# Performance work log

Measured on AMD Instinct MI355X. Metric: run time of the kernel, lower is better.

## Reference

```python
import jax, jax.numpy as jnp
import numpy as np

B, A, D, F, BF = 256, 128, 8, 512, 16  # batch, max_atoms, max_degree, atom_feat, bond_feat


def setup_inputs() -> dict:
    key = jax.random.key(0)
    k1, k2, k3 = jax.random.split(key, 3)
    atoms = jax.random.normal(k1, (B, A, F), dtype=jnp.float32)
    bonds = jax.random.normal(k2, (B, A, D, BF), dtype=jnp.float32)
    # -1 is the padding value for missing neighbours (as in the original layer)
    edges = jax.random.randint(k3, (B, A, D), -1, A, dtype=jnp.int32)
    return {"atoms": atoms, "bonds": bonds, "edges": edges}


def reference(atoms, bonds, edges):
    # atoms: (B, A, F); edges: (B, A, D) with -1 padding; bonds unused by this layer
    b, a, f = atoms.shape
    # neighbour_lookup with maskvalue=-inf: prepend a -inf row so index 0 (= edge -1 + 1) maps to mask
    pad = jnp.full((b, 1, f), -jnp.inf, dtype=atoms.dtype)
    masked_atoms = jnp.concatenate([pad, atoms], axis=1)        # (B, A+1, F)
    masked_edges = edges + 1                                     # (B, A, D), in [0, A]
    neigh = masked_atoms[jnp.arange(b)[:, None, None], masked_edges]  # (B, A, D, F)
    # include_self=True: prepend each atom's own features
    all_feats = jnp.concatenate([atoms[:, :, None, :], neigh], axis=2)  # (B, A, D+1, F)
    max_features = jnp.max(all_feats, axis=2)                   # (B, A, F)
    atom_degrees = jnp.sum(edges != -1, axis=-1, keepdims=True)  # (B, A, 1)
    general_atom_mask = (atom_degrees != 0).astype(atoms.dtype)
    return max_features * general_atom_mask
```

## Files before the change

kernel.cpp:

```cpp
#include <hip/hip_runtime.h>

#define B_ 256
#define A_ 128
#define D_ 8
#define F_ 512
#define NXCD 8

typedef float  vfloat4 __attribute__((ext_vector_type(4)));
typedef int    vint4   __attribute__((ext_vector_type(4)));

__global__ __launch_bounds__(128) void NeuralGraphPool_kernel(
    const float* __restrict__ atoms,
    const int*   __restrict__ edges,
    float*       __restrict__ out)
{
    const int hw  = blockIdx.x;
    const int blk = (hw & (NXCD - 1)) * ((B_ * A_) / NXCD) + (hw >> 3);

    const int b   = blk >> 7;
    const int a   = blk & (A_ - 1);
    const int t   = threadIdx.x;
    const int col = t * 4;

    const float* __restrict__ abase = atoms + (size_t)b * (A_ * F_);

    const int* ep = edges + (size_t)blk * D_;
    const vint4 e01 = *reinterpret_cast<const vint4*>(ep);
    const vint4 e23 = *reinterpret_cast<const vint4*>(ep + 4);
    int e[D_] = { e01.x, e01.y, e01.z, e01.w, e23.x, e23.y, e23.z, e23.w };

    int degree = 0;
#pragma unroll
    for (int d = 0; d < D_; ++d) degree += (e[d] >= 0) ? 1 : 0;

    vfloat4 acc = *reinterpret_cast<const vfloat4*>(abase + a * F_ + col);

#pragma unroll
    for (int d = 0; d < D_; ++d) {
        const int row = (e[d] >= 0) ? e[d] : a;
        const vfloat4 v = *reinterpret_cast<const vfloat4*>(abase + row * F_ + col);
        acc.x = fmaxf(acc.x, v.x);
        acc.y = fmaxf(acc.y, v.y);
        acc.z = fmaxf(acc.z, v.z);
        acc.w = fmaxf(acc.w, v.w);
    }

    vfloat4 r = acc;
    if (degree == 0) { r = (vfloat4)(0.f); }
    __builtin_nontemporal_store(r, reinterpret_cast<vfloat4*>(out + (size_t)blk * F_ + col));
}

extern "C" void kernel_launch(void* const* d_in, const int* in_sizes, int n_in,
                              void* d_out, int out_size, void* d_ws, size_t ws_size,
                              hipStream_t stream) {
    const float* atoms = (const float*)d_in[0];
    const int*   edges = (const int*)d_in[2];
    float*       out   = (float*)d_out;

    dim3 grid(B_ * A_);
    dim3 block(128);
    hipLaunchKernelGGL(NeuralGraphPool_kernel, grid, block, 0, stream,
                       atoms, edges, out);
}
```

Measured before the change: 31.01 us.

## Stage per-molecule feature slabs in LDS and gather neighbours from shared memory

Each block now handles one molecule and a 64-feature column chunk. It copies that 128x64 slab of atoms, plus the molecule's edge list, into shared memory, then computes the neighbour max for all atoms from LDS. Before, every atom block gathered up to 9 rows from global memory (mostly L2 hits), so this removes redundant global reads. In exchange it adds a __syncthreads, uses about 36KB of LDS per block, which limits occupancy, and may cause LDS bank conflicts from the irregular row gathers.

```diff
diff --git a/kernel.cpp b/kernel.cpp
--- a/kernel.cpp
+++ b/kernel.cpp
@@ -4,50 +4,77 @@
 #define A_ 128
 #define D_ 8
 #define F_ 512
+#define FC 64
+#define NCHUNK (F_ / FC)
+#define THREADS 256
 #define NXCD 8
 
-typedef float  vfloat4 __attribute__((ext_vector_type(4)));
-typedef int    vint4   __attribute__((ext_vector_type(4)));
+typedef float vfloat4 __attribute__((ext_vector_type(4)));
+typedef int   vint4   __attribute__((ext_vector_type(4)));
 
-__global__ __launch_bounds__(128) void NeuralGraphPool_kernel(
+__global__ __launch_bounds__(THREADS) void NeuralGraphPool_kernel(
     const float* __restrict__ atoms,
     const int*   __restrict__ edges,
     float*       __restrict__ out)
 {
+    __shared__ float slab[A_ * FC];
+    __shared__ int   eds[A_ * D_];
+
     const int hw  = blockIdx.x;
-    const int blk = (hw & (NXCD - 1)) * ((B_ * A_) / NXCD) + (hw >> 3);
+    const int blk = (hw & (NXCD - 1)) * ((B_ * NCHUNK) / NXCD) + (hw >> 3);
 
-    const int b   = blk >> 7;
-    const int a   = blk & (A_ - 1);
+    const int b   = blk >> 3;
+    const int fc0 = (blk & (NCHUNK - 1)) * FC;
     const int t   = threadIdx.x;
-    const int col = t * 4;
 
-    const float* __restrict__ abase = atoms + (size_t)b * (A_ * F_);
+    const float* __restrict__ abase = atoms + (size_t)b * (A_ * F_) + fc0;
 
-    const int* ep = edges + (size_t)blk * D_;
-    const vint4 e01 = *reinterpret_cast<const vint4*>(ep);
-    const vint4 e23 = *reinterpret_cast<const vint4*>(ep + 4);
-    int e[D_] = { e01.x, e01.y, e01.z, e01.w, e23.x, e23.y, e23.z, e23.w };
-
-    int degree = 0;
-#pragma unroll
-    for (int d = 0; d < D_; ++d) degree += (e[d] >= 0) ? 1 : 0;
-
-    vfloat4 acc = *reinterpret_cast<const vfloat4*>(abase + a * F_ + col);
+    {
+        const vint4 ev = *reinterpret_cast<const vint4*>(
+            edges + (size_t)b * (A_ * D_) + t * 4);
+        *reinterpret_cast<vint4*>(eds + t * 4) = ev;
+    }
 
 #pragma unroll
-    for (int d = 0; d < D_; ++d) {
-        const int row = (e[d] >= 0) ? e[d] : a;
-        const vfloat4 v = *reinterpret_cast<const vfloat4*>(abase + row * F_ + col);
-        acc.x = fmaxf(acc.x, v.x);
-        acc.y = fmaxf(acc.y, v.y);
-        acc.z = fmaxf(acc.z, v.z);
-        acc.w = fmaxf(acc.w, v.w);
+    for (int j = 0; j < (A_ * FC / 4) / THREADS; ++j) {
+        const int fi = j * THREADS + t;
+        const int a  = fi >> 4;
+        const int c  = fi & 15;
+        const vfloat4 v = *reinterpret_cast<const vfloat4*>(abase + a * F_ + c * 4);
+        *reinterpret_cast<vfloat4*>(slab + fi * 4) = v;
     }
+    __syncthreads();
 
-    vfloat4 r = acc;
-    if (degree == 0) { r = (vfloat4)(0.f); }
-    __builtin_nontemporal_store(r, reinterpret_cast<vfloat4*>(out + (size_t)blk * F_ + col));
+#pragma unroll 2
+    for (int k = 0; k < (A_ * FC / 4) / THREADS; ++k) {
+        const int o = k * THREADS + t;
+        const int a = o >> 4;
+        const int c = (o & 15) * 4;
+
+        int e[D_];
+        int degree = 0;
+#pragma unroll
+        for (int d = 0; d < D_; ++d) {
+            e[d] = eds[a * D_ + d];
+            degree += (e[d] >= 0) ? 1 : 0;
+        }
+
+        vfloat4 acc = *reinterpret_cast<const vfloat4*>(slab + a * FC + c);
+#pragma unroll
+        for (int d = 0; d < D_; ++d) {
+            const int row = (e[d] >= 0) ? e[d] : a;
+            const vfloat4 v = *reinterpret_cast<const vfloat4*>(slab + row * FC + c);
+            acc.x = fmaxf(acc.x, v.x);
+            acc.y = fmaxf(acc.y, v.y);
+            acc.z = fmaxf(acc.z, v.z);
+            acc.w = fmaxf(acc.w, v.w);
+        }
+
+        vfloat4 r = acc;
+        if (degree == 0) r = (vfloat4)(0.f);
+        __builtin_nontemporal_store(r, reinterpret_cast<vfloat4*>(
+            out + (size_t)b * (A_ * F_) + a * F_ + fc0 + c));
+    }
 }
 
 extern "C" void kernel_launch(void* const* d_in, const int* in_sizes, int n_in,
@@ -57,8 +84,8 @@
     const int*   edges = (const int*)d_in[2];
     float*       out   = (float*)d_out;
 
-    dim3 grid(B_ * A_);
-    dim3 block(128);
+    dim3 grid(B_ * NCHUNK);
+    dim3 block(THREADS);
     hipLaunchKernelGGL(NeuralGraphPool_kernel, grid, block, 0, stream,
                        atoms, edges, out);
 }
```

New measurement: 25.67 us. -17.2%, faster.
